# Kernel tuning notes

Hardware: AMD Instinct MI355X
Metric: run time of the kernel (lower is better)

Reference implementation:

```python
import jax, jax.numpy as jnp
import numpy as np
from jax import lax

B, N, C, T = 32, 1000, 32, 24
K, F_CHEB, F_TIME = 3, 64, 64


def setup_inputs() -> dict:
    key = jax.random.key(0)
    ks = jax.random.split(key, 7)
    return {
        "x": jax.random.normal(ks[0], (B, N, C, T), dtype=jnp.float32),
        "cheb_T": jax.random.normal(ks[1], (K, N, N), dtype=jnp.float32) * (1.0 / np.sqrt(N)),
        "Theta": jax.random.normal(ks[2], (K, C, F_CHEB), dtype=jnp.float32) * 0.1,
        "time_w": jax.random.normal(ks[3], (F_TIME, F_CHEB, 1, 3), dtype=jnp.float32) * 0.05,
        "time_b": jax.random.normal(ks[4], (F_TIME,), dtype=jnp.float32) * 0.05,
        "res_w": jax.random.normal(ks[5], (F_TIME, C, 1, 1), dtype=jnp.float32) * 0.1,
        "res_b": jax.random.normal(ks[6], (F_TIME,), dtype=jnp.float32) * 0.05,
    }


def _conv2d(x, w, stride_t, pad_t):
    # x: [B, Cin, N, T] (NCHW with H=nodes, W=time), w: [Cout, Cin, kh, kw]
    return lax.conv_general_dilated(
        x, w, window_strides=(1, stride_t), padding=((0, 0), (pad_t, pad_t)),
        dimension_numbers=("NCHW", "OIHW", "NCHW"))


def reference(x, cheb_T, Theta, time_w, time_b, res_w, res_b):
    # ChebConv: rhs_k[b,n,c,t] = sum_m T_k[m,n] x[b,m,c,t]; out = sum_k rhs_k @ Theta_k
    # Fused over all timesteps and polynomial orders in one einsum.
    spatial = jax.nn.relu(
        jnp.einsum("knm,bmct,kcf->bnft", cheb_T, x, Theta))  # [B,N,F_cheb,T]
    # time conv over the T axis (kernel (1,3), pad (0,1), stride (1,1))
    h = spatial.transpose(0, 2, 1, 3)  # [B,F_cheb,N,T]
    tc = _conv2d(h, time_w, 1, 1) + time_b[None, :, None, None]
    tc = jnp.tanh(tc) * jax.nn.sigmoid(tc)  # wave-net gating
    # 1x1 residual conv on the raw input (Dropout output in source is unused)
    res = _conv2d(x.transpose(0, 2, 1, 3), res_w, 1, 0) + res_b[None, :, None, None]
    out = (res + tc).transpose(0, 2, 1, 3)  # [B,N,F_time,T]
    return out
```

## Files before the change

### kernel.cpp

```cpp
#include <hip/hip_runtime.h>
#include <math.h>

typedef __attribute__((ext_vector_type(4))) float f32x4;
typedef __attribute__((ext_vector_type(16))) float f32x16;
typedef __attribute__((ext_vector_type(8))) short s16x8;
typedef __attribute__((ext_vector_type(8))) unsigned short u16x8;
typedef __attribute__((ext_vector_type(4))) unsigned short u16x4;

#define NB 32
#define NN 1000
#define NT 24
#define NP 1024
#define TCN 768

#define GLOAD16(g, l) __builtin_amdgcn_global_load_lds( \
    (const __attribute__((address_space(1))) unsigned int*)(g), \
    (__attribute__((address_space(3))) unsigned int*)(l), 16, 0, 0)

__device__ __forceinline__ unsigned short f2bf(float f){
  union { float fv; unsigned int u; } v; v.fv = f;
  unsigned int r = v.u + 0x7FFFu + ((v.u >> 16) & 1u);
  return (unsigned short)(r >> 16);
}

__global__ void k0_cheb(const float* __restrict__ cheb, unsigned short* __restrict__ cbT){
  int idx = blockIdx.x * 256 + threadIdx.x;
  int base = idx << 2;
  int m = base & (NP - 1);
  int r = base >> 10;
  int n = r & (NP - 1);
  int k = r >> 10;
  u16x4 o = (u16x4){0,0,0,0};
  if (n < NN && m < NN){
    if (m + 3 < NN){
      f32x4 v = *(const f32x4*)(cheb + ((size_t)k*NN + n)*NN + m);
      o[0] = f2bf(v[0]); o[1] = f2bf(v[1]); o[2] = f2bf(v[2]); o[3] = f2bf(v[3]);
    } else {
      #pragma unroll
      for (int i = 0; i < 4; ++i)
        if (m + i < NN) o[i] = f2bf(cheb[((size_t)k*NN + n)*NN + m + i]);
    }
  }
  *(u16x4*)(cbT + base) = o;
}

__global__ __launch_bounds__(256) void k0_x(const float* __restrict__ x,
                     unsigned short* __restrict__ xbT, unsigned short* __restrict__ xt2){
  __shared__ unsigned short tile[64*770];
  const int b  = blockIdx.x >> 4;
  const int m0 = (blockIdx.x & 15) << 6;
  const int tid = threadIdx.x;
  for (int i = tid; i < 64*192; i += 256){
    int mi = i / 192, c4 = (i - mi*192) << 2;
    f32x4 v = (f32x4){0.f,0.f,0.f,0.f};
    if (m0 + mi < NN) v = *(const f32x4*)(x + (size_t)(b*NN + m0 + mi)*768 + c4);
    unsigned short* tp = tile + mi*770 + c4;
    tp[0] = f2bf(v[0]); tp[1] = f2bf(v[1]); tp[2] = f2bf(v[2]); tp[3] = f2bf(v[3]);
  }
  __syncthreads();
  {
    const int seg = tid & 7, r0 = tid >> 3;
    for (int rr = 0; rr < 768; rr += 32){
      int r = rr + r0;
      int t = r >> 5, c = r & 31, ct = c*24 + t;
      u16x8 v;
      #pragma unroll
      for (int e = 0; e < 8; ++e) v[e] = tile[(seg*8 + e)*770 + ct];
      *(u16x8*)(xbT + ((size_t)b*TCN + r)*NP + m0 + seg*8) = v;
    }
  }
  if (m0 < NN){
    int rows = NN - m0; if (rows > 64) rows = 64;
    for (int i = tid; i < rows*96; i += 256){
      int mi = i / 96, s = i - mi*96;
      u16x8 v;
      #pragma unroll
      for (int e = 0; e < 8; ++e){
        int r = s*8 + e; int t = r >> 5, c = r & 31;
        v[e] = tile[mi*770 + c*24 + t];
      }
      *(u16x8*)(xt2 + (size_t)(b*NN + m0 + mi)*TCN + s*8) = v;
    }
  }
}

__global__ void k0_w(const float* __restrict__ Theta, const float* __restrict__ tw,
                     const float* __restrict__ rw,
                     unsigned short* __restrict__ ThT, unsigned short* __restrict__ WtT,
                     unsigned short* __restrict__ rwT){
  int i = blockIdx.x * 256 + threadIdx.x;
  if (i < 64*96){
    int f = i / 96, kc = i - f*96;
    ThT[i] = f2bf(Theta[kc*64 + f]);
  }
  if (i < 64*192){
    int f = i / 192, kk = i - f*192;
    int dt = kk >> 6, fi = kk & 63;
    WtT[i] = f2bf(tw[(f*64 + fi)*3 + dt]);
  }
  if (i < 64*32){
    rwT[i] = f2bf(rw[i]);
  }
}

__global__ __launch_bounds__(256, 2) void k1_cheb_theta(
    const unsigned short* __restrict__ cbT,
    const unsigned short* __restrict__ xbT,
    const unsigned short* __restrict__ ThT,
    unsigned short* __restrict__ spa)
{
  __shared__ __align__(16) unsigned short smem[30720];

  int pB = blockIdx.x;
  int lb = (pB & 7) * 384 + (pB >> 3);
  const int tcb = lb % 6; lb /= 6;
  const int nt  = lb & 15;
  const int b   = lb >> 4;

  const int tid  = threadIdx.x;
  const int wid  = tid >> 6;
  const int lane = tid & 63;
  const int l31  = lane & 31;
  const int h    = lane >> 5;
  const int wr   = wid >> 1;
  const int wc   = wid & 1;

  const int rl4 = lane >> 2;
  const int swz = (((lane & 3) ^ ((rl4 >> 1) & 3)) << 3);
  const unsigned short* baseA = cbT + (size_t)(nt*64 + rl4)*NP + swz;
  const unsigned short* baseB = xbT + ((size_t)b*TCN + tcb*128 + rl4)*NP + swz;
  char* smc = (char*)smem;

  const int s_rd = (l31 >> 1) & 3;
  const int ch0 = ((h ^ s_rd) << 3);
  const int ch1 = (((2 + h) ^ s_rd) << 3);

  f32x16 acc[3][2];
  #pragma unroll
  for (int k = 0; k < 3; ++k)
    #pragma unroll
    for (int j = 0; j < 2; ++j)
      #pragma unroll
      for (int r = 0; r < 16; ++r) acc[k][j][r] = 0.f;

  const int rA  = wr*32 + l31;
  const int rB0 = wc*64 + l31;

  auto stage = [&](int step, int buf){
    const int so = step << 5;
    const int bo = buf * 20480;
    #pragma unroll
    for (int q = 0; q < 5; ++q){
      const int g = wid*5 + q;
      if (g < 12){
        const int k = g >> 2, rg = g & 3;
        GLOAD16(baseA + (size_t)k*NP*NP + rg*16*NP + so, smc + bo + k*4096 + rg*1024);
      } else {
        const int rg = g - 12;
        GLOAD16(baseB + (size_t)rg*16*NP + so, smc + bo + 12288 + rg*1024);
      }
    }
  };

  stage(0, 0);
  stage(1, 1);
  asm volatile("s_waitcnt vmcnt(5)" ::: "memory");
  __builtin_amdgcn_s_barrier();

  int cur = 0, pre = 2;
  for (int step = 0; step < 32; ++step){
    if (step < 30) stage(step + 2, pre);
    const unsigned short* sb = smem + cur*10240;
    #pragma unroll
    for (int ks = 0; ks < 2; ++ks){
      const int ch = ks ? ch1 : ch0;
      s16x8 bf0 = *(const s16x8*)(sb + 6144 + rB0*32 + ch);
      s16x8 bf1 = *(const s16x8*)(sb + 6144 + (rB0 + 32)*32 + ch);
      s16x8 af0 = *(const s16x8*)(sb +        rA*32 + ch);
      s16x8 af1 = *(const s16x8*)(sb + 2048 + rA*32 + ch);
      s16x8 af2 = *(const s16x8*)(sb + 4096 + rA*32 + ch);
      __builtin_amdgcn_s_setprio(1);
      acc[0][0] = __builtin_amdgcn_mfma_f32_32x32x16_bf16(af0, bf0, acc[0][0], 0, 0, 0);
      acc[0][1] = __builtin_amdgcn_mfma_f32_32x32x16_bf16(af0, bf1, acc[0][1], 0, 0, 0);
      acc[1][0] = __builtin_amdgcn_mfma_f32_32x32x16_bf16(af1, bf0, acc[1][0], 0, 0, 0);
      acc[1][1] = __builtin_amdgcn_mfma_f32_32x32x16_bf16(af1, bf1, acc[1][1], 0, 0, 0);
      acc[2][0] = __builtin_amdgcn_mfma_f32_32x32x16_bf16(af2, bf0, acc[2][0], 0, 0, 0);
      acc[2][1] = __builtin_amdgcn_mfma_f32_32x32x16_bf16(af2, bf1, acc[2][1], 0, 0, 0);
      __builtin_amdgcn_s_setprio(0);
    }
    if (step < 30)       asm volatile("s_waitcnt vmcnt(5)" ::: "memory");
    else if (step == 30) asm volatile("s_waitcnt vmcnt(0)" ::: "memory");
    __builtin_amdgcn_s_barrier();
    cur = (cur == 2) ? 0 : cur + 1;
    pre = (pre == 2) ? 0 : pre + 1;
  }

  s16x8 b2[3][2];
  const int fE = wc*32 + l31;
  #pragma unroll
  for (int ch = 0; ch < 3; ++ch)
    #pragma unroll
    for (int ks = 0; ks < 2; ++ks)
      b2[ch][ks] = *(const s16x8*)(ThT + fE*96 + ch*32 + ks*16 + h*8);

  unsigned short* yl = smem;
  const int rowE = wr*32 + l31;
  #pragma unroll
  for (int p = 0; p < 4; ++p){
    __syncthreads();
    if (wc == (p >> 1)){
      const int jj = p & 1;
      #pragma unroll
      for (int k = 0; k < 3; ++k)
        #pragma unroll
        for (int r = 0; r < 16; ++r){
          const int nl = wr*32 + (r & 3) + ((r >> 2) << 3) + (h << 2);
          const int kc = k*32 + l31;
          const int q  = kc >> 3;
          yl[nl*104 + (((q ^ (nl & 3)) << 3) | (kc & 7))] = f2bf(acc[k][jj][r]);
        }
    }
    __syncthreads();
    f32x16 a2c;
    #pragma unroll
    for (int r = 0; r < 16; ++r) a2c[r] = 0.f;
    #pragma unroll
    for (int ch = 0; ch < 3; ++ch)
      #pragma unroll
      for (int ks = 0; ks < 2; ++ks){
        const int q = ch*4 + ks*2 + h;
        s16x8 a2 = *(const s16x8*)(yl + rowE*104 + ((q ^ (rowE & 3)) << 3));
        a2c = __builtin_amdgcn_mfma_f32_32x32x16_bf16(a2, b2[ch][ks], a2c, 0, 0, 0);
      }
    const int t = tcb*4 + p;
    #pragma unroll
    for (int r = 0; r < 16; ++r){
      const int nl = wr*32 + (r & 3) + ((r >> 2) << 3) + (h << 2);
      const int n  = nt*64 + nl;
      if (n < NN)
        spa[((size_t)(b*NN + n)*NT + t)*64 + fE] = f2bf(fmaxf(a2c[r], 0.f));
    }
  }
}

__global__ __launch_bounds__(256, 2) void k2_out(
    const unsigned short* __restrict__ spa, const unsigned short* __restrict__ xt2,
    const unsigned short* __restrict__ WtT, const unsigned short* __restrict__ rwT,
    const float* __restrict__ tb, const float* __restrict__ rb,
    float* __restrict__ out)
{
  __shared__ __align__(16) unsigned short sst[36864];
  const unsigned short* spa_s = sst;
  const unsigned short* xt2_s = sst + 24576;

  const int c0   = blockIdx.x * 16;
  const int tid  = threadIdx.x;
  const int w    = tid >> 6;
  const int lane = tid & 63;
  const int l31  = lane & 31;
  const int h    = lane >> 5;
  char* smc = (char*)sst;

  const unsigned short* gs = spa + (size_t)c0 * 1536;
  const unsigned short* gx = xt2 + (size_t)c0 * 768;
  #pragma unroll
  for (int it = 0; it < 12; ++it){
    const int row = it*32 + (tid >> 3);
    const int sc  = (tid & 7) ^ (row & 7);
    GLOAD16(gs + (size_t)row*64 + sc*8, smc + it*4096 + w*1024);
  }
  #pragma unroll
  for (int it = 0; it < 6; ++it){
    const int row = it*64 + (tid >> 2);
    const int sc  = (tid & 3) ^ ((row >> 1) & 3);
    GLOAD16(gx + (size_t)row*32 + sc*8, smc + 49152 + it*4096 + w*1024);
  }
  __syncthreads();

  const float tb0v = tb[l31], tb1v = tb[32 + l31];
  const float rb0v = rb[l31], rb1v = rb[32 + l31];

  #pragma unroll
  for (int g = 0; g < 3; ++g){
    const int rbase = w*96 + g*32;
    const int r = rbase + l31;
    const int cell = r / 24;
    const int t = r - cell*24;

    f32x16 a0, a1, rs0, rs1;
    #pragma unroll
    for (int e = 0; e < 16; ++e){ a0[e]=0.f; a1[e]=0.f; rs0[e]=0.f; rs1[e]=0.f; }

    #pragma unroll
    for (int s = 0; s < 12; ++s){
      const int dt = s >> 2;
      const int tv = t + dt - 1;
      int ar = r + dt - 1;
      ar = ar < 0 ? 0 : (ar > 383 ? 383 : ar);
      const int cfi = ((s & 3) << 1) + h;
      s16x8 a = *(const s16x8*)(spa_s + (size_t)ar*64 + ((cfi ^ (ar & 7)) << 3));
      if (!((unsigned)tv < 24u)) a = (s16x8){0,0,0,0,0,0,0,0};
      s16x8 b0 = *(const s16x8*)(WtT + (size_t)l31*192 + s*16 + h*8);
      s16x8 b1 = *(const s16x8*)(WtT + (size_t)(32 + l31)*192 + s*16 + h*8);
      a0 = __builtin_amdgcn_mfma_f32_32x32x16_bf16(a, b0, a0, 0, 0, 0);
      a1 = __builtin_amdgcn_mfma_f32_32x32x16_bf16(a, b1, a1, 0, 0, 0);
    }
    #pragma unroll
    for (int s = 0; s < 2; ++s){
      const int cres = (s << 1) + h;
      s16x8 a = *(const s16x8*)(xt2_s + (size_t)r*32 + ((cres ^ ((r >> 1) & 3)) << 3));
      s16x8 b0 = *(const s16x8*)(rwT + (size_t)l31*32 + s*16 + h*8);
      s16x8 b1 = *(const s16x8*)(rwT + (size_t)(32 + l31)*32 + s*16 + h*8);
      rs0 = __builtin_amdgcn_mfma_f32_32x32x16_bf16(a, b0, rs0, 0, 0, 0);
      rs1 = __builtin_amdgcn_mfma_f32_32x32x16_bf16(a, b1, rs1, 0, 0, 0);
    }

    #pragma unroll
    for (int q = 0; q < 4; ++q){
      const int rq = rbase + q*8 + 4*h;
      const int cq = rq / 24;
      const int tq = rq - cq*24;
      f32x4 v0, v1;
      #pragma unroll
      for (int e = 0; e < 4; ++e){
        float z0 = a0[q*4 + e] + tb0v;
        float e0 = __expf(-z0);
        v0[e] = rs0[q*4 + e] + rb0v + (1.f - e0) * __builtin_amdgcn_rcpf(1.f + e0*e0);
        float z1 = a1[q*4 + e] + tb1v;
        float e1 = __expf(-z1);
        v1[e] = rs1[q*4 + e] + rb1v + (1.f - e1) * __builtin_amdgcn_rcpf(1.f + e1*e1);
      }
      *(f32x4*)(out + ((size_t)(c0 + cq)*64 + l31)*24 + tq)      = v0;
      *(f32x4*)(out + ((size_t)(c0 + cq)*64 + 32 + l31)*24 + tq) = v1;
    }
  }
}

extern "C" void kernel_launch(void* const* d_in, const int* in_sizes, int n_in,
                              void* d_out, int out_size, void* d_ws, size_t ws_size,
                              hipStream_t stream) {
  const float* x     = (const float*)d_in[0];
  const float* cheb  = (const float*)d_in[1];
  const float* Theta = (const float*)d_in[2];
  const float* tw    = (const float*)d_in[3];
  const float* tb    = (const float*)d_in[4];
  const float* rw    = (const float*)d_in[5];
  const float* rb    = (const float*)d_in[6];
  float* out = (float*)d_out;

  char* ws = (char*)d_ws;
  size_t off = 0;
  auto alloc = [&](size_t bytes) -> void* {
    void* p = ws + off;
    off += (bytes + 255) & ~(size_t)255;
    return p;
  };
  unsigned short* cbT = (unsigned short*)alloc((size_t)3*NP*NP*2);
  unsigned short* xbT = (unsigned short*)alloc((size_t)NB*TCN*NP*2);
  unsigned short* xt2 = (unsigned short*)alloc((size_t)NB*NN*TCN*2);
  unsigned short* spa = (unsigned short*)alloc((size_t)NB*NN*NT*64*2);
  unsigned short* ThT = (unsigned short*)alloc((size_t)64*96*2);
  unsigned short* WtT = (unsigned short*)alloc((size_t)64*192*2);
  unsigned short* rwT = (unsigned short*)alloc((size_t)64*32*2);

  hipLaunchKernelGGL(k0_cheb, dim3(3072), dim3(256), 0, stream, cheb, cbT);
  hipLaunchKernelGGL(k0_x,    dim3(512),  dim3(256), 0, stream, x, xbT, xt2);
  hipLaunchKernelGGL(k0_w,    dim3(48),   dim3(256), 0, stream, Theta, tw, rw, ThT, WtT, rwT);
  hipLaunchKernelGGL(k1_cheb_theta, dim3(32*16*6), dim3(256), 0, stream, cbT, xbT, ThT, spa);
  hipLaunchKernelGGL(k2_out,  dim3(2000), dim3(256), 0, stream, spa, xt2, WtT, rwT, tb, rb, out);
}
```

Baseline: 396.4 us.

## Load Chebyshev operand directly into registers and stage only x through LDS

The GEMM main loop no longer stages the three Chebyshev A-tiles through LDS. Each wave now loads its own A fragments from global memory into registers, double-buffered one step ahead, and only the x (B) tiles keep the triple-buffered LDS path. This shrinks the shared-memory footprint and cuts LDS write and read traffic per step. In exchange, the two waves that share the same A rows both fetch them from global memory, the per-lane global reads are strided, the setprio hints are dropped, and the epilogue's reuse of the smaller smem buffer may be tight.

```diff
diff --git a/kernel.cpp b/kernel.cpp
--- a/kernel.cpp
+++ b/kernel.cpp
@@ -109,7 +109,7 @@
     const unsigned short* __restrict__ ThT,
     unsigned short* __restrict__ spa)
 {
-  __shared__ __align__(16) unsigned short smem[30720];
+  __shared__ __align__(16) unsigned short smem[12288];
 
   int pB = blockIdx.x;
   int lb = (pB & 7) * 384 + (pB >> 3);
@@ -125,15 +125,26 @@
   const int wr   = wid >> 1;
   const int wc   = wid & 1;
 
-  const int rl4 = lane >> 2;
-  const int swz = (((lane & 3) ^ ((rl4 >> 1) & 3)) << 3);
-  const unsigned short* baseA = cbT + (size_t)(nt*64 + rl4)*NP + swz;
-  const unsigned short* baseB = xbT + ((size_t)b*TCN + tcb*128 + rl4)*NP + swz;
+  const int rl4b = lane >> 2;
+  const int swzb = (((lane & 3) ^ ((rl4b >> 1) & 3)) << 3);
+  const unsigned short* baseB = xbT + ((size_t)b*TCN + tcb*128 + rl4b)*NP + swzb;
   char* smc = (char*)smem;
+  auto stageB = [&](int step, int buf){
+    const int so = step << 5;
+    const int bo = buf * 8192;
+    #pragma unroll
+    for (int q = 0; q < 2; ++q){
+      const int g = wid*2 + q;
+      GLOAD16(baseB + (size_t)g*16*NP + so, smc + bo + g*1024);
+    }
+  };
+
+  const unsigned short* gA = cbT + (size_t)(nt*64 + wr*32 + l31)*NP + h*8;
 
   const int s_rd = (l31 >> 1) & 3;
   const int ch0 = ((h ^ s_rd) << 3);
   const int ch1 = (((2 + h) ^ s_rd) << 3);
+  const int rB0 = wc*64 + l31;
 
   f32x16 acc[3][2];
   #pragma unroll
@@ -143,52 +154,55 @@
       #pragma unroll
       for (int r = 0; r < 16; ++r) acc[k][j][r] = 0.f;
 
-  const int rA  = wr*32 + l31;
-  const int rB0 = wc*64 + l31;
-
-  auto stage = [&](int step, int buf){
-    const int so = step << 5;
-    const int bo = buf * 20480;
-    #pragma unroll
-    for (int q = 0; q < 5; ++q){
-      const int g = wid*5 + q;
-      if (g < 12){
-        const int k = g >> 2, rg = g & 3;
-        GLOAD16(baseA + (size_t)k*NP*NP + rg*16*NP + so, smc + bo + k*4096 + rg*1024);
-      } else {
-        const int rg = g - 12;
-        GLOAD16(baseB + (size_t)rg*16*NP + so, smc + bo + 12288 + rg*1024);
-      }
-    }
-  };
-
-  stage(0, 0);
-  stage(1, 1);
-  asm volatile("s_waitcnt vmcnt(5)" ::: "memory");
+  stageB(0, 0);
+  stageB(1, 1);
+  s16x8 cA00 = *(const s16x8*)(gA);
+  s16x8 cA01 = *(const s16x8*)(gA + 16);
+  s16x8 cA10 = *(const s16x8*)(gA + (size_t)NP*NP);
+  s16x8 cA11 = *(const s16x8*)(gA + (size_t)NP*NP + 16);
+  s16x8 cA20 = *(const s16x8*)(gA + (size_t)2*NP*NP);
+  s16x8 cA21 = *(const s16x8*)(gA + (size_t)2*NP*NP + 16);
+  asm volatile("s_waitcnt vmcnt(0)" ::: "memory");
   __builtin_amdgcn_s_barrier();
 
   int cur = 0, pre = 2;
   for (int step = 0; step < 32; ++step){
-    if (step < 30) stage(step + 2, pre);
-    const unsigned short* sb = smem + cur*10240;
-    #pragma unroll
-    for (int ks = 0; ks < 2; ++ks){
-      const int ch = ks ? ch1 : ch0;
-      s16x8 bf0 = *(const s16x8*)(sb + 6144 + rB0*32 + ch);
-      s16x8 bf1 = *(const s16x8*)(sb + 6144 + (rB0 + 32)*32 + ch);
-      s16x8 af0 = *(const s16x8*)(sb +        rA*32 + ch);
-      s16x8 af1 = *(const s16x8*)(sb + 2048 + rA*32 + ch);
-      s16x8 af2 = *(const s16x8*)(sb + 4096 + rA*32 + ch);
-      __builtin_amdgcn_s_setprio(1);
-      acc[0][0] = __builtin_amdgcn_mfma_f32_32x32x16_bf16(af0, bf0, acc[0][0], 0, 0, 0);
-      acc[0][1] = __builtin_amdgcn_mfma_f32_32x32x16_bf16(af0, bf1, acc[0][1], 0, 0, 0);
-      acc[1][0] = __builtin_amdgcn_mfma_f32_32x32x16_bf16(af1, bf0, acc[1][0], 0, 0, 0);
-      acc[1][1] = __builtin_amdgcn_mfma_f32_32x32x16_bf16(af1, bf1, acc[1][1], 0, 0, 0);
-      acc[2][0] = __builtin_amdgcn_mfma_f32_32x32x16_bf16(af2, bf0, acc[2][0], 0, 0, 0);
-      acc[2][1] = __builtin_amdgcn_mfma_f32_32x32x16_bf16(af2, bf1, acc[2][1], 0, 0, 0);
-      __builtin_amdgcn_s_setprio(0);
-    }
-    if (step < 30)       asm volatile("s_waitcnt vmcnt(5)" ::: "memory");
+    s16x8 nA00, nA01, nA10, nA11, nA20, nA21;
+    if (step < 31){
+      const int so = (step + 1) << 5;
+      nA00 = *(const s16x8*)(gA + so);
+      nA01 = *(const s16x8*)(gA + so + 16);
+      nA10 = *(const s16x8*)(gA + (size_t)NP*NP + so);
+      nA11 = *(const s16x8*)(gA + (size_t)NP*NP + so + 16);
+      nA20 = *(const s16x8*)(gA + (size_t)2*NP*NP + so);
+      nA21 = *(const s16x8*)(gA + (size_t)2*NP*NP + so + 16);
+    }
+    if (step < 30) stageB(step + 2, pre);
+
+    const unsigned short* sb = smem + cur*4096;
+    {
+      s16x8 bf0 = *(const s16x8*)(sb + rB0*32 + ch0);
+      s16x8 bf1 = *(const s16x8*)(sb + (rB0 + 32)*32 + ch0);
+      acc[0][0] = __builtin_amdgcn_mfma_f32_32x32x16_bf16(cA00, bf0, acc[0][0], 0, 0, 0);
+      acc[0][1] = __builtin_amdgcn_mfma_f32_32x32x16_bf16(cA00, bf1, acc[0][1], 0, 0, 0);
+      acc[1][0] = __builtin_amdgcn_mfma_f32_32x32x16_bf16(cA10, bf0, acc[1][0], 0, 0, 0);
+      acc[1][1] = __builtin_amdgcn_mfma_f32_32x32x16_bf16(cA10, bf1, acc[1][1], 0, 0, 0);
+      acc[2][0] = __builtin_amdgcn_mfma_f32_32x32x16_bf16(cA20, bf0, acc[2][0], 0, 0, 0);
+      acc[2][1] = __builtin_amdgcn_mfma_f32_32x32x16_bf16(cA20, bf1, acc[2][1], 0, 0, 0);
+    }
+    {
+      s16x8 bf0 = *(const s16x8*)(sb + rB0*32 + ch1);
+      s16x8 bf1 = *(const s16x8*)(sb + (rB0 + 32)*32 + ch1);
+      acc[0][0] = __builtin_amdgcn_mfma_f32_32x32x16_bf16(cA01, bf0, acc[0][0], 0, 0, 0);
+      acc[0][1] = __builtin_amdgcn_mfma_f32_32x32x16_bf16(cA01, bf1, acc[0][1], 0, 0, 0);
+      acc[1][0] = __builtin_amdgcn_mfma_f32_32x32x16_bf16(cA11, bf0, acc[1][0], 0, 0, 0);
+      acc[1][1] = __builtin_amdgcn_mfma_f32_32x32x16_bf16(cA11, bf1, acc[1][1], 0, 0, 0);
+      acc[2][0] = __builtin_amdgcn_mfma_f32_32x32x16_bf16(cA21, bf0, acc[2][0], 0, 0, 0);
+      acc[2][1] = __builtin_amdgcn_mfma_f32_32x32x16_bf16(cA21, bf1, acc[2][1], 0, 0, 0);
+    }
+    cA00 = nA00; cA01 = nA01; cA10 = nA10; cA11 = nA11; cA20 = nA20; cA21 = nA21;
+
+    if (step < 30)       asm volatile("s_waitcnt vmcnt(2)" ::: "memory");
     else if (step == 30) asm volatile("s_waitcnt vmcnt(0)" ::: "memory");
     __builtin_amdgcn_s_barrier();
     cur = (cur == 2) ? 0 : cur + 1;
```

New measurement: 553.6 us. 39.6% more time.

## Give each wave a private double-buffered LDS tile to drop block barriers

Applied to the files above, without the earlier changes.

The Chebyshev GEMM main loop previously staged a shared block tile into three LDS buffers, with a block-wide barrier every K step. Now each wave loads its own A rows and B columns into a private double-buffered LDS region and relies only on per-wave vmcnt waits, so the per-step barriers go away. In exchange, A and B tiles are fetched redundantly by the waves that share them, which raises global and L2 traffic and the number of load instructions. LDS use grows to 80 KB, and prefetch depth drops from two steps to one.

```diff
diff --git a/kernel.cpp b/kernel.cpp
--- a/kernel.cpp
+++ b/kernel.cpp
@@ -109,7 +109,7 @@
     const unsigned short* __restrict__ ThT,
     unsigned short* __restrict__ spa)
 {
-  __shared__ __align__(16) unsigned short smem[30720];
+  __shared__ __align__(16) unsigned short smem[40960];
 
   int pB = blockIdx.x;
   int lb = (pB & 7) * 384 + (pB >> 3);
@@ -127,9 +127,22 @@
 
   const int rl4 = lane >> 2;
   const int swz = (((lane & 3) ^ ((rl4 >> 1) & 3)) << 3);
-  const unsigned short* baseA = cbT + (size_t)(nt*64 + rl4)*NP + swz;
-  const unsigned short* baseB = xbT + ((size_t)b*TCN + tcb*128 + rl4)*NP + swz;
+  const unsigned short* baseA = cbT + (size_t)(nt*64 + wr*32 + rl4)*NP + swz;
+  const unsigned short* baseB = xbT + ((size_t)b*TCN + tcb*128 + wc*64 + rl4)*NP + swz;
   char* smc = (char*)smem;
+
+  auto stage = [&](int step, int buf){
+    const int so = step << 5;
+    char* d = smc + buf*40960 + wid*10240;
+    #pragma unroll
+    for (int k = 0; k < 3; ++k)
+      #pragma unroll
+      for (int rg = 0; rg < 2; ++rg)
+        GLOAD16(baseA + (size_t)k*NP*NP + (size_t)rg*16*NP + so, d + k*2048 + rg*1024);
+    #pragma unroll
+    for (int rg = 0; rg < 4; ++rg)
+      GLOAD16(baseB + (size_t)rg*16*NP + so, d + 6144 + rg*1024);
+  };
 
   const int s_rd = (l31 >> 1) & 3;
   const int ch0 = ((h ^ s_rd) << 3);
@@ -143,42 +156,23 @@
       #pragma unroll
       for (int r = 0; r < 16; ++r) acc[k][j][r] = 0.f;
 
-  const int rA  = wr*32 + l31;
-  const int rB0 = wc*64 + l31;
-
-  auto stage = [&](int step, int buf){
-    const int so = step << 5;
-    const int bo = buf * 20480;
-    #pragma unroll
-    for (int q = 0; q < 5; ++q){
-      const int g = wid*5 + q;
-      if (g < 12){
-        const int k = g >> 2, rg = g & 3;
-        GLOAD16(baseA + (size_t)k*NP*NP + rg*16*NP + so, smc + bo + k*4096 + rg*1024);
-      } else {
-        const int rg = g - 12;
-        GLOAD16(baseB + (size_t)rg*16*NP + so, smc + bo + 12288 + rg*1024);
-      }
-    }
-  };
-
   stage(0, 0);
-  stage(1, 1);
-  asm volatile("s_waitcnt vmcnt(5)" ::: "memory");
-  __builtin_amdgcn_s_barrier();
-
-  int cur = 0, pre = 2;
+
+  int cur = 0;
   for (int step = 0; step < 32; ++step){
-    if (step < 30) stage(step + 2, pre);
-    const unsigned short* sb = smem + cur*10240;
-    #pragma unroll
-    for (int ks = 0; ks < 2; ++ks){
-      const int ch = ks ? ch1 : ch0;
-      s16x8 bf0 = *(const s16x8*)(sb + 6144 + rB0*32 + ch);
-      s16x8 bf1 = *(const s16x8*)(sb + 6144 + (rB0 + 32)*32 + ch);
-      s16x8 af0 = *(const s16x8*)(sb +        rA*32 + ch);
-      s16x8 af1 = *(const s16x8*)(sb + 2048 + rA*32 + ch);
-      s16x8 af2 = *(const s16x8*)(sb + 4096 + rA*32 + ch);
+    if (step < 31){
+      stage(step + 1, cur ^ 1);
+      asm volatile("s_waitcnt vmcnt(10)" ::: "memory");
+    } else {
+      asm volatile("s_waitcnt vmcnt(0)" ::: "memory");
+    }
+    const unsigned short* wb = smem + cur*20480 + wid*5120;
+    {
+      s16x8 af0 = *(const s16x8*)(wb +        l31*32 + ch0);
+      s16x8 af1 = *(const s16x8*)(wb + 1024 + l31*32 + ch0);
+      s16x8 af2 = *(const s16x8*)(wb + 2048 + l31*32 + ch0);
+      s16x8 bf0 = *(const s16x8*)(wb + 3072 + l31*32 + ch0);
+      s16x8 bf1 = *(const s16x8*)(wb + 3072 + (32 + l31)*32 + ch0);
       __builtin_amdgcn_s_setprio(1);
       acc[0][0] = __builtin_amdgcn_mfma_f32_32x32x16_bf16(af0, bf0, acc[0][0], 0, 0, 0);
       acc[0][1] = __builtin_amdgcn_mfma_f32_32x32x16_bf16(af0, bf1, acc[0][1], 0, 0, 0);
@@ -188,12 +182,25 @@
       acc[2][1] = __builtin_amdgcn_mfma_f32_32x32x16_bf16(af2, bf1, acc[2][1], 0, 0, 0);
       __builtin_amdgcn_s_setprio(0);
     }
-    if (step < 30)       asm volatile("s_waitcnt vmcnt(5)" ::: "memory");
-    else if (step == 30) asm volatile("s_waitcnt vmcnt(0)" ::: "memory");
-    __builtin_amdgcn_s_barrier();
-    cur = (cur == 2) ? 0 : cur + 1;
-    pre = (pre == 2) ? 0 : pre + 1;
-  }
+    {
+      s16x8 af0 = *(const s16x8*)(wb +        l31*32 + ch1);
+      s16x8 af1 = *(const s16x8*)(wb + 1024 + l31*32 + ch1);
+      s16x8 af2 = *(const s16x8*)(wb + 2048 + l31*32 + ch1);
+      s16x8 bf0 = *(const s16x8*)(wb + 3072 + l31*32 + ch1);
+      s16x8 bf1 = *(const s16x8*)(wb + 3072 + (32 + l31)*32 + ch1);
+      __builtin_amdgcn_s_setprio(1);
+      acc[0][0] = __builtin_amdgcn_mfma_f32_32x32x16_bf16(af0, bf0, acc[0][0], 0, 0, 0);
+      acc[0][1] = __builtin_amdgcn_mfma_f32_32x32x16_bf16(af0, bf1, acc[0][1], 0, 0, 0);
+      acc[1][0] = __builtin_amdgcn_mfma_f32_32x32x16_bf16(af1, bf0, acc[1][0], 0, 0, 0);
+      acc[1][1] = __builtin_amdgcn_mfma_f32_32x32x16_bf16(af1, bf1, acc[1][1], 0, 0, 0);
+      acc[2][0] = __builtin_amdgcn_mfma_f32_32x32x16_bf16(af2, bf0, acc[2][0], 0, 0, 0);
+      acc[2][1] = __builtin_amdgcn_mfma_f32_32x32x16_bf16(af2, bf1, acc[2][1], 0, 0, 0);
+      __builtin_amdgcn_s_setprio(0);
+    }
+    cur ^= 1;
+  }
+
+  __syncthreads();
 
   s16x8 b2[3][2];
   const int fE = wc*32 + l31;
```

After: 427.8 us. 1.08x slower.
